# Kernel optimization log

Hardware: AMD Instinct MI355X
Metric: run time of the kernel (lower is better)

Reference implementation:

```python
import jax, jax.numpy as jnp
import numpy as np

WEIGHT_GT = 0.004
WEIGHT_BG = 0.0002
STRIDES = (8, 16, 32, 64, 128)
SIZES = (128, 64, 32, 16, 8)
B, C, N = 8, 256, 16


def setup_inputs() -> dict:
    key = jax.random.key(0)
    ks = jax.random.split(key, 32)
    inp = {}
    for i, hw in enumerate(SIZES):
        inp[f"feat_s{i}"] = jax.random.normal(ks[i], (B, C, hw, hw), jnp.float32)
        inp[f"feat_t{i}"] = jax.random.normal(ks[5 + i], (B, C, hw, hw), jnp.float32)
        inp[f"adapt_w{i}"] = jax.random.normal(ks[10 + i], (C, C), jnp.float32) * 0.05
        inp[f"adapt_b{i}"] = jnp.zeros((C,), jnp.float32)
    # valid boxes: x1<x2, y1<y2, inside a 1024px image
    x1 = jax.random.uniform(ks[20], (B, N), minval=0.0, maxval=800.0)
    y1 = jax.random.uniform(ks[21], (B, N), minval=0.0, maxval=800.0)
    bw = jax.random.uniform(ks[22], (B, N), minval=8.0, maxval=224.0)
    bh = jax.random.uniform(ks[23], (B, N), minval=8.0, maxval=224.0)
    inp["gt_bboxes"] = jnp.stack([x1, y1, x1 + bw, y1 + bh], axis=-1)  # [B,N,4]
    return inp


def gt_mask(gt_bboxes, h, w, stride):
    """Vectorized rasterization of the nested-loop mask builder. [B,N,4] -> [B,h,w]."""
    q = jnp.floor(gt_bboxes / stride).astype(jnp.int32)  # int() truncation (coords >= 0)
    lx = jnp.minimum(q[..., 0], w - 1)[:, :, None, None]  # [B,N,1,1]
    ly = jnp.minimum(q[..., 1], h - 1)[:, :, None, None]
    rx = jnp.minimum(q[..., 2], w - 1)[:, :, None, None]
    ry = jnp.minimum(q[..., 3], h - 1)[:, :, None, None]
    Y = jnp.arange(h)[:, None]  # [h,1]
    X = jnp.arange(w)[None, :]  # [1,w]
    degenerate = (lx == rx) | (ly == ry)
    inside = (Y >= ly) & (Y < ry) & (X >= lx) & (X < rx)   # slice ly:ry, lx:rx
    point = (Y == ly) & (X == lx)                          # single-pixel fallback
    per_box = jnp.where(degenerate, point, inside)         # [B,N,h,w]
    return jnp.any(per_box, axis=1).astype(jnp.float32)    # (mask > 0)


def _level_loss(feat_t, feat_s, w, b, gt_bboxes, stride):
    # 1x1-conv adaptation layer
    adapted = jnp.einsum('bchw,oc->bohw', feat_s, w) + b[None, :, None, None]
    h, wd = feat_t.shape[2], feat_t.shape[3]
    mask = gt_mask(gt_bboxes, h, wd, stride)[:, None, :, :]  # [B,1,H,W]
    diff = (feat_t - adapted) ** 2
    s_gt = jnp.sum(diff * mask)
    s_bg = jnp.sum(diff * (1.0 - mask))
    loss_gt = jnp.sqrt(s_gt + 1e-8)
    loss_bg = jnp.sqrt(s_bg + 1e-8)
    return WEIGHT_GT * loss_gt + WEIGHT_BG * loss_bg


def reference(feat_s0, feat_t0, adapt_w0, adapt_b0,
              feat_s1, feat_t1, adapt_w1, adapt_b1,
              feat_s2, feat_t2, adapt_w2, adapt_b2,
              feat_s3, feat_t3, adapt_w3, adapt_b3,
              feat_s4, feat_t4, adapt_w4, adapt_b4,
              gt_bboxes):
    fs = (feat_s0, feat_s1, feat_s2, feat_s3, feat_s4)
    ft = (feat_t0, feat_t1, feat_t2, feat_t3, feat_t4)
    ws = (adapt_w0, adapt_w1, adapt_w2, adapt_w3, adapt_w4)
    bs = (adapt_b0, adapt_b1, adapt_b2, adapt_b3, adapt_b4)
    loss = jnp.float32(0.0)
    for i in range(5):  # fixed, small number of pyramid levels
        loss = loss + _level_loss(ft[i], fs[i], ws[i], bs[i], gt_bboxes, STRIDES[i])
    return loss
```

## Files before the change

### kernel.cpp

```cpp
#include <hip/hip_runtime.h>
#include <math.h>

typedef __attribute__((ext_vector_type(8))) short short8;
typedef __attribute__((ext_vector_type(4))) float floatx4;

__device__ __forceinline__ short f2bf(float f) {
  union { float f; unsigned u; } v; v.f = f;
  unsigned r = v.u + 0x7fffu + ((v.u >> 16) & 1u);
  return (short)(r >> 16);
}

struct Params {
  const float* fs[5];
  const float* ft[5];
  const float* bias[5];
  const float* mask[5];
  const short8* wp[5];
  float* sums;
};

__global__ void prep(const float* __restrict__ w0, const float* __restrict__ w1,
                     const float* __restrict__ w2, const float* __restrict__ w3,
                     const float* __restrict__ w4, short8* __restrict__ wp,
                     const float* __restrict__ gtb, float* __restrict__ mask_base,
                     float* __restrict__ sums) {
  __shared__ int lx[16], ly[16], rx[16], ry[16], dg[16];
  int blk = blockIdx.x;
  if (blk < 160) {
    int id = blk * 256 + threadIdx.x;
    int lvl = id >> 13;
    int idx = id & 8191;
    const float* W = (lvl == 0) ? w0 : (lvl == 1) ? w1 : (lvl == 2) ? w2 : (lvl == 3) ? w3 : w4;
    int t16 = idx >> 9;
    int kt  = (idx >> 6) & 7;
    int ln  = idx & 63;
    int m = t16 * 16 + (ln & 15);
    int c = kt * 32 + (ln >> 4) * 8;
    const float* s = W + m * 256 + c;
    short8 v;
#pragma unroll
    for (int j = 0; j < 8; j++) v[j] = f2bf(s[j]);
    wp[id] = v;
  } else if (blk < 200) {
    const int szs[5]  = {128, 64, 32, 16, 8};
    const int strd[5] = {8, 16, 32, 64, 128};
    const int offs[5] = {0, 131072, 163840, 172032, 174080};
    int idx = blk - 160;
    int b = idx & 7, lvl = idx >> 3;
    int hw = szs[lvl];
    int P = hw * hw;
    if (threadIdx.x < 16) {
      int n = threadIdx.x;
      const float* bb = gtb + (b * 16 + n) * 4;
      float inv = 1.0f / (float)strd[lvl];
      int qx1 = (int)floorf(bb[0] * inv);
      int qy1 = (int)floorf(bb[1] * inv);
      int qx2 = (int)floorf(bb[2] * inv);
      int qy2 = (int)floorf(bb[3] * inv);
      int wl = hw - 1;
      int a = min(qx1, wl), c = min(qy1, wl), d = min(qx2, wl), e = min(qy2, wl);
      lx[n] = a; ly[n] = c; rx[n] = d; ry[n] = e;
      dg[n] = (a == d) || (c == e);
    }
    __syncthreads();
    float* mp = mask_base + offs[lvl] + b * P;
    for (int p = threadIdx.x; p < P; p += blockDim.x) {
      int y = p / hw, x = p - y * hw;
      bool any = false;
#pragma unroll
      for (int n = 0; n < 16; n++) {
        bool cov = dg[n] ? (y == ly[n] && x == lx[n])
                         : (y >= ly[n] && y < ry[n] && x >= lx[n] && x < rx[n]);
        any = any || cov;
      }
      mp[p] = any ? 1.0f : 0.0f;
    }
  } else {
    if (threadIdx.x < 16) sums[threadIdx.x] = 0.f;
  }
}

template<int PL2, int LVL>
__device__ __forceinline__ void level_body(const Params& pr, int rem, float* red,
                                           short8 (*lbuf)[64][4]) {
  constexpr int P = 64 << PL2;
  const int tid  = threadIdx.x;
  const int lane = tid & 63;
  const int wave = tid >> 6;
  const int quad = lane >> 4, l15 = lane & 15;
  const int bz = rem >> PL2;
  const int p0 = (rem & ((1 << PL2) - 1)) << 6;

  const float*  fsb   = pr.fs[LVL]  + (size_t)bz * 256 * P;
  const float*  ftb   = pr.ft[LVL]  + (size_t)bz * 256 * P;
  const short8* wpb   = pr.wp[LVL]  + lane;
  const float*  maskb = pr.mask[LVL] + (size_t)bz * P;
  const float*  biasp = pr.bias[LVL];

  const float* gbase = fsb + (size_t)quad * 8 * P + (p0 + wave * 16 + l15);

  floatx4 acc[4][4];
#pragma unroll
  for (int i = 0; i < 4; i++)
#pragma unroll
    for (int j = 0; j < 4; j++) acc[i][j] = (floatx4){0.f, 0.f, 0.f, 0.f};

  float  g[2][8];
  short8 af[2][4];

#pragma unroll
  for (int j = 0; j < 8; j++) g[0][j] = gbase[(size_t)(0 * 32 + j) * P];
#pragma unroll
  for (int mi = 0; mi < 4; mi++) af[0][mi] = wpb[((wave * 4 + mi) * 8 + 0) * 64];
#pragma unroll
  for (int j = 0; j < 8; j++) g[1][j] = gbase[(size_t)(1 * 32 + j) * P];
  {
    short8 v;
#pragma unroll
    for (int j = 0; j < 8; j++) v[j] = f2bf(g[0][j]);
    lbuf[0][wave * 16 + l15][quad] = v;
  }
  asm volatile("s_waitcnt lgkmcnt(0)" ::: "memory");
  __builtin_amdgcn_s_barrier();
  asm volatile("" ::: "memory");

#pragma unroll
  for (int kt = 0; kt < 8; kt++) {
    const int cur = kt & 1;
    float  gn[8];
    short8 afn[4];
    if (kt + 2 < 8) {
#pragma unroll
      for (int j = 0; j < 8; j++) gn[j] = gbase[(size_t)((kt + 2) * 32 + j) * P];
    }
    if (kt + 1 < 8) {
#pragma unroll
      for (int mi = 0; mi < 4; mi++)
        afn[mi] = wpb[((wave * 4 + mi) * 8 + (kt + 1)) * 64];
    }

    short8 bf[4];
#pragma unroll
    for (int ni = 0; ni < 4; ni++) bf[ni] = lbuf[cur][ni * 16 + l15][quad];
#pragma unroll
    for (int mi = 0; mi < 4; mi++)
#pragma unroll
      for (int ni = 0; ni < 4; ni++)
        acc[mi][ni] = __builtin_amdgcn_mfma_f32_16x16x32_bf16(af[cur][mi], bf[ni], acc[mi][ni], 0, 0, 0);

    if (kt + 1 < 8) {
      short8 v;
#pragma unroll
      for (int j = 0; j < 8; j++) v[j] = f2bf(g[1 - cur][j]);
      lbuf[1 - cur][wave * 16 + l15][quad] = v;
#pragma unroll
      for (int mi = 0; mi < 4; mi++) af[1 - cur][mi] = afn[mi];
    }
    if (kt + 2 < 8) {
#pragma unroll
      for (int j = 0; j < 8; j++) g[cur][j] = gn[j];
    }
    if (kt + 1 < 8) {
      asm volatile("s_waitcnt lgkmcnt(0)" ::: "memory");
      __builtin_amdgcn_s_barrier();
      asm volatile("" ::: "memory");
    }
  }

  float sgt = 0.f, sbg = 0.f;
#pragma unroll
  for (int ni = 0; ni < 4; ni++) {
    int p = p0 + ni * 16 + l15;
    float mk = maskb[p];
#pragma unroll
    for (int mi = 0; mi < 4; mi++) {
      int ob = wave * 64 + mi * 16 + quad * 4;
      const float* ftp = ftb + (size_t)ob * P + p;
#pragma unroll
      for (int r = 0; r < 4; r++) {
        float ad = acc[mi][ni][r] + biasp[ob + r];
        float tv = ftp[(size_t)r * P];
        float d = tv - ad;
        float sq = d * d;
        sgt += sq * mk;
        sbg += sq - sq * mk;
      }
    }
  }
#pragma unroll
  for (int off = 32; off > 0; off >>= 1) {
    sgt += __shfl_down(sgt, off);
    sbg += __shfl_down(sbg, off);
  }
  if (lane == 0) { red[wave * 2] = sgt; red[wave * 2 + 1] = sbg; }
  __syncthreads();
  if (tid == 0) {
    atomicAdd(&pr.sums[LVL * 2 + 0], red[0] + red[2] + red[4] + red[6]);
    atomicAdd(&pr.sums[LVL * 2 + 1], red[1] + red[3] + red[5] + red[7]);
  }
}

__global__ __launch_bounds__(256, 2) void gemm_loss_all(Params pr) {
  __shared__ short8 lbuf[2][64][4];
  __shared__ float red[8];
  int id = blockIdx.x;
  if (id < 2048)      level_body<8, 0>(pr, id,        red, lbuf);
  else if (id < 2560) level_body<6, 1>(pr, id - 2048, red, lbuf);
  else if (id < 2688) level_body<4, 2>(pr, id - 2560, red, lbuf);
  else if (id < 2720) level_body<2, 3>(pr, id - 2688, red, lbuf);
  else                level_body<0, 4>(pr, id - 2720, red, lbuf);
}

__global__ void finalize(const float* __restrict__ sums, float* __restrict__ out) {
  if (threadIdx.x == 0 && blockIdx.x == 0) {
    float L = 0.f;
#pragma unroll
    for (int i = 0; i < 5; i++)
      L += 0.004f * sqrtf(sums[2 * i] + 1e-8f) + 0.0002f * sqrtf(sums[2 * i + 1] + 1e-8f);
    out[0] = L;
  }
}

extern "C" void kernel_launch(void* const* d_in, const int* in_sizes, int n_in,
                              void* d_out, int out_size, void* d_ws, size_t ws_size,
                              hipStream_t stream) {
  (void)in_sizes; (void)n_in; (void)out_size; (void)ws_size;
  const float* fs[5]; const float* ftp[5]; const float* aw[5]; const float* ab[5];
  for (int i = 0; i < 5; i++) {
    fs[i]  = (const float*)d_in[4 * i + 0];
    ftp[i] = (const float*)d_in[4 * i + 1];
    aw[i]  = (const float*)d_in[4 * i + 2];
    ab[i]  = (const float*)d_in[4 * i + 3];
  }
  const float* gtb = (const float*)d_in[20];
  float* out = (float*)d_out;
  char* ws = (char*)d_ws;

  float*  sums  = (float*)ws;
  float*  masks = (float*)(ws + 64);
  short8* wp    = (short8*)(ws + 64 + 698368);

  prep<<<201, 256, 0, stream>>>(aw[0], aw[1], aw[2], aw[3], aw[4], wp, gtb, masks, sums);

  const int moff[5] = {0, 131072, 163840, 172032, 174080};
  Params pr;
  for (int l = 0; l < 5; l++) {
    pr.fs[l]   = fs[l];
    pr.ft[l]   = ftp[l];
    pr.bias[l] = ab[l];
    pr.mask[l] = masks + moff[l];
    pr.wp[l]   = wp + l * 8192;
  }
  pr.sums = sums;

  gemm_loss_all<<<2728, 256, 0, stream>>>(pr);
  finalize<<<1, 64, 0, stream>>>(sums, out);
}
```

Before: 444.9 us.

## Use 1024-thread blocks with coalesced row loads staged through LDS transpose

Blocks become 1024 threads covering 256-pixel strips. Each wave loads contiguous 64-pixel rows of two channels (coalesced) and writes them into a padded fp32 LDS tile, replacing the old scattered per-lane channel-strided loads. The epilogue also stages accumulators through LDS so teacher features are read row-contiguously. This is meant to cut memory-access inefficiency, at the cost of more barriers, more LDS traffic, and fp32-to-bf16 conversions repeated per wave.

```diff
diff --git a/kernel.cpp b/kernel.cpp
--- a/kernel.cpp
+++ b/kernel.cpp
@@ -80,87 +80,111 @@
   }
 }
 
-template<int PL2, int LVL>
-__device__ __forceinline__ void level_body(const Params& pr, int rem, float* red,
-                                           short8 (*lbuf)[64][4]) {
+template<int PL2, int SL2, int LVL>
+__device__ __forceinline__ void level_body(const Params& pr, int rem, float* smem) {
   constexpr int P = 64 << PL2;
+  constexpr int PSTRIP = 64 << SL2;
+  constexpr int NI = PSTRIP / 64;
+  constexpr int ROUNDS = PSTRIP / 64;
+  constexpr int STRIPS = P / PSTRIP;
+
   const int tid  = threadIdx.x;
   const int lane = tid & 63;
-  const int wave = tid >> 6;
+  const int w    = tid >> 6;
   const int quad = lane >> 4, l15 = lane & 15;
-  const int bz = rem >> PL2;
-  const int p0 = (rem & ((1 << PL2) - 1)) << 6;
-
-  const float*  fsb   = pr.fs[LVL]  + (size_t)bz * 256 * P;
-  const float*  ftb   = pr.ft[LVL]  + (size_t)bz * 256 * P;
-  const short8* wpb   = pr.wp[LVL]  + lane;
-  const float*  maskb = pr.mask[LVL] + (size_t)bz * P;
-  const float*  biasp = pr.bias[LVL];
-
-  const float* gbase = fsb + (size_t)quad * 8 * P + (p0 + wave * 16 + l15);
-
-  floatx4 acc[4][4];
-#pragma unroll
-  for (int i = 0; i < 4; i++)
-#pragma unroll
-    for (int j = 0; j < 4; j++) acc[i][j] = (floatx4){0.f, 0.f, 0.f, 0.f};
-
-  float  g[2][8];
-  short8 af[2][4];
-
-#pragma unroll
-  for (int j = 0; j < 8; j++) g[0][j] = gbase[(size_t)(0 * 32 + j) * P];
-#pragma unroll
-  for (int mi = 0; mi < 4; mi++) af[0][mi] = wpb[((wave * 4 + mi) * 8 + 0) * 64];
-#pragma unroll
-  for (int j = 0; j < 8; j++) g[1][j] = gbase[(size_t)(1 * 32 + j) * P];
-  {
-    short8 v;
-#pragma unroll
-    for (int j = 0; j < 8; j++) v[j] = f2bf(g[0][j]);
-    lbuf[0][wave * 16 + l15][quad] = v;
-  }
+  const int wq   = w >> 2;
+  const int p_off = (w & 3) * (PSTRIP / 4);
+
+  const int bz = rem / STRIPS;
+  const int p0 = (rem % STRIPS) * PSTRIP;
+
+  float* tb0  = smem;
+  float* tb1  = smem + 8704;
+  float* mbuf = smem + 17408;
+  float* red  = smem + 17664;
+  float* cbuf = smem;
+
+  const float* fsb   = pr.fs[LVL] + (size_t)bz * 256 * P + p0 + lane;
+  const float* ftbp  = pr.ft[LVL] + (size_t)bz * 256 * P + p0 + lane;
+  const float* maskb = pr.mask[LVL] + (size_t)bz * P + p0;
+  const float* biasp = pr.bias[LVL];
+  const short8* wpb  = pr.wp[LVL] + wq * 2048 + lane;
+
+  if (tid < PSTRIP) mbuf[tid] = maskb[tid];
+
+  const int c0 = 2 * w;
+
+  float sv[2][2][ROUNDS];
+#pragma unroll
+  for (int h = 0; h < 2; ++h) {
+    const float* rp = fsb + (size_t)(c0 + h) * P;
+#pragma unroll
+    for (int r = 0; r < ROUNDS; ++r) sv[0][h][r] = rp[r * 64];
+  }
+#pragma unroll
+  for (int h = 0; h < 2; ++h) {
+    const float* rp = fsb + (size_t)(32 + c0 + h) * P;
+#pragma unroll
+    for (int r = 0; r < ROUNDS; ++r) sv[1][h][r] = rp[r * 64];
+  }
+#pragma unroll
+  for (int h = 0; h < 2; ++h)
+#pragma unroll
+    for (int r = 0; r < ROUNDS; ++r)
+      tb0[(r * 64 + lane) * 34 + c0 + h] = sv[0][h][r];
   asm volatile("s_waitcnt lgkmcnt(0)" ::: "memory");
   __builtin_amdgcn_s_barrier();
   asm volatile("" ::: "memory");
 
-#pragma unroll
-  for (int kt = 0; kt < 8; kt++) {
-    const int cur = kt & 1;
-    float  gn[8];
-    short8 afn[4];
-    if (kt + 2 < 8) {
-#pragma unroll
-      for (int j = 0; j < 8; j++) gn[j] = gbase[(size_t)((kt + 2) * 32 + j) * P];
-    }
-    if (kt + 1 < 8) {
-#pragma unroll
-      for (int mi = 0; mi < 4; mi++)
-        afn[mi] = wpb[((wave * 4 + mi) * 8 + (kt + 1)) * 64];
-    }
-
-    short8 bf[4];
-#pragma unroll
-    for (int ni = 0; ni < 4; ni++) bf[ni] = lbuf[cur][ni * 16 + l15][quad];
-#pragma unroll
-    for (int mi = 0; mi < 4; mi++)
-#pragma unroll
-      for (int ni = 0; ni < 4; ni++)
-        acc[mi][ni] = __builtin_amdgcn_mfma_f32_16x16x32_bf16(af[cur][mi], bf[ni], acc[mi][ni], 0, 0, 0);
-
-    if (kt + 1 < 8) {
+  floatx4 acc[4][NI];
+#pragma unroll
+  for (int i = 0; i < 4; ++i)
+#pragma unroll
+    for (int j = 0; j < NI; ++j) acc[i][j] = (floatx4){0.f, 0.f, 0.f, 0.f};
+
+#pragma unroll
+  for (int kt = 0; kt < 8; ++kt) {
+    const int cur = kt & 1, nxt = cur ^ 1;
+    if (kt < 6) {
+#pragma unroll
+      for (int h = 0; h < 2; ++h) {
+        const float* rp = fsb + (size_t)((kt + 2) * 32 + c0 + h) * P;
+#pragma unroll
+        for (int r = 0; r < ROUNDS; ++r) sv[cur][h][r] = rp[r * 64];
+      }
+    }
+    short8 af[4];
+#pragma unroll
+    for (int mi = 0; mi < 4; ++mi) af[mi] = wpb[(mi * 8 + kt) * 64];
+
+    const float* tbc = cur ? tb1 : tb0;
+    short8 bf[NI];
+#pragma unroll
+    for (int ni = 0; ni < NI; ++ni) {
+      int pl = p_off + ni * 16 + l15;
+      const float2* q2 = (const float2*)(tbc + pl * 34 + quad * 8);
       short8 v;
 #pragma unroll
-      for (int j = 0; j < 8; j++) v[j] = f2bf(g[1 - cur][j]);
-      lbuf[1 - cur][wave * 16 + l15][quad] = v;
-#pragma unroll
-      for (int mi = 0; mi < 4; mi++) af[1 - cur][mi] = afn[mi];
-    }
-    if (kt + 2 < 8) {
-#pragma unroll
-      for (int j = 0; j < 8; j++) g[cur][j] = gn[j];
-    }
-    if (kt + 1 < 8) {
+      for (int g = 0; g < 4; ++g) {
+        float2 x = q2[g];
+        v[2 * g]     = f2bf(x.x);
+        v[2 * g + 1] = f2bf(x.y);
+      }
+      bf[ni] = v;
+    }
+#pragma unroll
+    for (int mi = 0; mi < 4; ++mi)
+#pragma unroll
+      for (int ni = 0; ni < NI; ++ni)
+        acc[mi][ni] = __builtin_amdgcn_mfma_f32_16x16x32_bf16(af[mi], bf[ni], acc[mi][ni], 0, 0, 0);
+
+    if (kt < 7) {
+      float* tbn = nxt ? tb1 : tb0;
+#pragma unroll
+      for (int h = 0; h < 2; ++h)
+#pragma unroll
+        for (int r = 0; r < ROUNDS; ++r)
+          tbn[(r * 64 + lane) * 34 + c0 + h] = sv[nxt][h][r];
       asm volatile("s_waitcnt lgkmcnt(0)" ::: "memory");
       __builtin_amdgcn_s_barrier();
       asm volatile("" ::: "memory");
@@ -169,46 +193,73 @@
 
   float sgt = 0.f, sbg = 0.f;
 #pragma unroll
-  for (int ni = 0; ni < 4; ni++) {
-    int p = p0 + ni * 16 + l15;
-    float mk = maskb[p];
-#pragma unroll
-    for (int mi = 0; mi < 4; mi++) {
-      int ob = wave * 64 + mi * 16 + quad * 4;
-      const float* ftp = ftb + (size_t)ob * P + p;
-#pragma unroll
-      for (int r = 0; r < 4; r++) {
-        float ad = acc[mi][ni][r] + biasp[ob + r];
-        float tv = ftp[(size_t)r * P];
-        float d = tv - ad;
+  for (int oc = 0; oc < 8; ++oc) {
+    asm volatile("s_waitcnt lgkmcnt(0)" ::: "memory");
+    __builtin_amdgcn_s_barrier();
+    asm volatile("" ::: "memory");
+    if (wq == (oc >> 1)) {
+      const int mb = 2 * (oc & 1);
+#pragma unroll
+      for (int m2 = 0; m2 < 2; ++m2)
+#pragma unroll
+        for (int ni = 0; ni < NI; ++ni) {
+          int pl = p_off + ni * 16 + l15;
+          float* cp = cbuf + pl * 34 + m2 * 16 + quad * 4;
+          floatx4 a = acc[mb + m2][ni];
+          ((float2*)cp)[0] = make_float2(a[0], a[1]);
+          ((float2*)(cp + 2))[0] = make_float2(a[2], a[3]);
+        }
+    }
+    float ftv[2][ROUNDS];
+#pragma unroll
+    for (int h = 0; h < 2; ++h) {
+      const float* rp = ftbp + (size_t)(oc * 32 + c0 + h) * P;
+#pragma unroll
+      for (int r = 0; r < ROUNDS; ++r) ftv[h][r] = rp[r * 64];
+    }
+    asm volatile("s_waitcnt lgkmcnt(0)" ::: "memory");
+    __builtin_amdgcn_s_barrier();
+    asm volatile("" ::: "memory");
+#pragma unroll
+    for (int h = 0; h < 2; ++h) {
+      float bv = biasp[oc * 32 + c0 + h];
+#pragma unroll
+      for (int r = 0; r < ROUNDS; ++r) {
+        int pl = r * 64 + lane;
+        float m = mbuf[pl];
+        float a = cbuf[pl * 34 + (c0 + h)] + bv;
+        float d = ftv[h][r] - a;
         float sq = d * d;
-        sgt += sq * mk;
-        sbg += sq - sq * mk;
+        sgt += sq * m;
+        sbg += sq - sq * m;
       }
     }
   }
+
 #pragma unroll
   for (int off = 32; off > 0; off >>= 1) {
     sgt += __shfl_down(sgt, off);
     sbg += __shfl_down(sbg, off);
   }
-  if (lane == 0) { red[wave * 2] = sgt; red[wave * 2 + 1] = sbg; }
+  if (lane == 0) { red[w * 2] = sgt; red[w * 2 + 1] = sbg; }
   __syncthreads();
   if (tid == 0) {
-    atomicAdd(&pr.sums[LVL * 2 + 0], red[0] + red[2] + red[4] + red[6]);
-    atomicAdd(&pr.sums[LVL * 2 + 1], red[1] + red[3] + red[5] + red[7]);
-  }
-}
-
-__global__ __launch_bounds__(256, 2) void gemm_loss_all(Params pr) {
-  __shared__ short8 lbuf[2][64][4];
-  __shared__ float red[8];
+    float a = 0.f, b = 0.f;
+#pragma unroll
+    for (int i = 0; i < 16; ++i) { a += red[2 * i]; b += red[2 * i + 1]; }
+    atomicAdd(&pr.sums[LVL * 2 + 0], a);
+    atomicAdd(&pr.sums[LVL * 2 + 1], b);
+  }
+}
+
+__global__ __launch_bounds__(1024, 4) void gemm_loss_all(Params pr) {
+  __shared__ float smem[17696];
   int id = blockIdx.x;
-  if (id < 2048)      level_body<8, 0>(pr, id,        red, lbuf);
-  else if (id < 2560) level_body<6, 1>(pr, id - 2048, red, lbuf);
-  else if (id < 2688) level_body<4, 2>(pr, id - 2560, red, lbuf);
-  else if (id < 2720) level_body<2, 3>(pr, id - 2688, red, lbuf);
-  else                level_body<0, 4>(pr, id - 2720, red, lbuf);
+  if (id < 512)      level_body<8, 2, 0>(pr, id,       smem);
+  else if (id < 640) level_body<6, 2, 1>(pr, id - 512, smem);
+  else if (id < 672) level_body<4, 2, 2>(pr, id - 640, smem);
+  else if (id < 680) level_body<2, 2, 3>(pr, id - 672, smem);
+  else               level_body<0, 0, 4>(pr, id - 680, smem);
 }
 
 __global__ void finalize(const float* __restrict__ sums, float* __restrict__ out) {
@@ -253,6 +304,6 @@
   }
   pr.sums = sums;
 
-  gemm_loss_all<<<2728, 256, 0, stream>>>(pr);
+  gemm_loss_all<<<688, 1024, 0, stream>>>(pr);
   finalize<<<1, 64, 0, stream>>>(sums, out);
 }
```

Result: slower. 677.8 us (+52.3%).
